# Kernel tuning notes

Hardware: AMD Instinct MI355X
Metric: run time of the kernel (lower is better)

Reference implementation:

```python
import jax, jax.numpy as jnp
import numpy as np

L, H, NH, DH, FF, V = 12, 768, 12, 64, 3072, 21128
B, S, TITLE = 64, 120, 20


def _ln(h, w, b):
    m = h.mean(-1, keepdims=True)
    v = ((h - m) ** 2).mean(-1, keepdims=True)
    return (h - m) * jax.lax.rsqrt(v + 1e-12) * w + b


def _prefix_causal_bias():
    # title tokens attend only to title; content tokens attend to title + causal content
    top = jnp.concatenate([jnp.ones((TITLE, TITLE)), jnp.zeros((TITLE, S - TITLE))], axis=1)
    bot = jnp.concatenate([jnp.ones((S - TITLE, TITLE)), jnp.tril(jnp.ones((S - TITLE, S - TITLE)))], axis=1)
    mask = jnp.concatenate([top, bot], axis=0)  # [S,S]
    return (1.0 - mask) * -1e9


def setup_inputs() -> dict:
    key = jax.random.key(0)
    ks = iter(jax.random.split(key, 32))

    def p(shape):
        return jax.random.normal(next(ks), shape, jnp.float32) * 0.02

    return {
        "x": jax.random.randint(next(ks), (B, S), 0, V),
        "y": jax.random.randint(next(ks), (B, S), 0, V),
        "word_emb": p((V, H)),
        "pos_emb": p((S, H)),
        "type_emb": p((1, H)),
        "emb_ln_w": jnp.ones((H,)), "emb_ln_b": jnp.zeros((H,)),
        "q_w": p((L, H, H)), "q_b": jnp.zeros((L, H)),
        "k_w": p((L, H, H)), "k_b": jnp.zeros((L, H)),
        "v_w": p((L, H, H)), "v_b": jnp.zeros((L, H)),
        "ao_w": p((L, H, H)), "ao_b": jnp.zeros((L, H)),
        "a_ln_w": jnp.ones((L, H)), "a_ln_b": jnp.zeros((L, H)),
        "f1_w": p((L, H, FF)), "f1_b": jnp.zeros((L, FF)),
        "f2_w": p((L, FF, H)), "f2_b": jnp.zeros((L, H)),
        "f_ln_w": jnp.ones((L, H)), "f_ln_b": jnp.zeros((L, H)),
        "cls_w": p((H, V)), "cls_b": jnp.zeros((V,)),
    }


def reference(x, y, word_emb, pos_emb, type_emb, emb_ln_w, emb_ln_b,
              q_w, q_b, k_w, k_b, v_w, v_b, ao_w, ao_b, a_ln_w, a_ln_b,
              f1_w, f1_b, f2_w, f2_b, f_ln_w, f_ln_b, cls_w, cls_b):
    bias = _prefix_causal_bias()[None, None]  # [1,1,S,S]
    h = _ln(word_emb[x] + pos_emb[None] + type_emb[0][None, None], emb_ln_w, emb_ln_b)

    def layer(h, pl):
        qw, qb, kw, kb, vw, vb, aow, aob, alw, alb, f1w, f1b, f2w, f2b, flw, flb = pl
        q = (h @ qw + qb).reshape(B, S, NH, DH)
        k = (h @ kw + kb).reshape(B, S, NH, DH)
        v = (h @ vw + vb).reshape(B, S, NH, DH)
        scores = jnp.einsum('bqhd,bkhd->bhqk', q, k) / np.float32(np.sqrt(DH)) + bias
        attn = jax.nn.softmax(scores, axis=-1)
        ctx = jnp.einsum('bhqk,bkhd->bqhd', attn, v).reshape(B, S, H)
        h = _ln(h + ctx @ aow + aob, alw, alb)
        ff = jax.nn.gelu(h @ f1w + f1b, approximate=False) @ f2w + f2b
        h = _ln(h + ff, flw, flb)
        return h, None

    h, _ = jax.lax.scan(layer, h, (q_w, q_b, k_w, k_b, v_w, v_b, ao_w, ao_b,
                                   a_ln_w, a_ln_b, f1_w, f1_b, f2_w, f2_b,
                                   f_ln_w, f_ln_b))
    logits = h @ cls_w + cls_b  # [B,S,V]
    logp = jax.nn.log_softmax(logits, axis=-1)
    nll = -jnp.take_along_axis(logp, y[..., None], axis=-1)[..., 0]
    return nll.mean()  # torch cross_entropy default reduction='mean'
```

## Files before the change

### kernel.cpp

```cpp
#include <hip/hip_runtime.h>
#include <hip/hip_bf16.h>
#include <hip/hip_fp16.h>
#include <cstdio>
#include <cstdint>

typedef __hip_bfloat16 bf16;
using bf16x8 = __attribute__((ext_vector_type(8))) __bf16;
using f32x4  = __attribute__((ext_vector_type(4))) float;

#define LNUM 12
#define HDIM 768
#define NHEAD 12
#define DHEAD 64
#define FFDIM 3072
#define VOCAB 21128
#define VPAD  21248
#define NBATCH 64
#define SEQ 120
#define TITLEN 20
#define MROWS (NBATCH*SEQ)
#define NTCLS (VPAD/128)

__device__ __forceinline__ float us2f(unsigned short u) {
  union { unsigned int u; float f; } c; c.u = ((unsigned int)u) << 16; return c.f;
}
__device__ __forceinline__ unsigned short f2us(float x) {
  bf16 h = __float2bfloat16(x);
  return *reinterpret_cast<unsigned short*>(&h);
}

template<int EPI>
__launch_bounds__(256, 4)
__global__ void gemm_bt(const bf16* __restrict__ A, const bf16* __restrict__ Bt,
                        const float* __restrict__ bias, bf16* __restrict__ C,
                        int N, int K, int nbx, int nby) {
  __shared__ __align__(16) unsigned short smA[2][128*32];
  __shared__ __align__(16) unsigned short smB[2][128*32];

  const int nwg = nbx * nby;
  const int orig = blockIdx.x;
  const int q8 = nwg >> 3, r8 = nwg & 7;
  const int xcd = orig & 7, lin = orig >> 3;
  const int pid = (xcd < r8 ? xcd * (q8 + 1) : r8 * (q8 + 1) + (xcd - r8) * q8) + lin;
  const int pg = 8 * nbx;
  const int g = pid / pg;
  const int rem = pid - g * pg;
  const int rows = min(8, nby - g * 8);
  const int by = g * 8 + rem % rows;
  const int bx = rem / rows;

  const int t = threadIdx.x;
  const int l = t & 63, w = t >> 6;
  const int wr = w >> 1, wc = w & 1;
  const int brow = by * 128;
  const int bcol = bx * 128;

  f32x4 acc[4][4];
#pragma unroll
  for (int i = 0; i < 4; ++i)
#pragma unroll
    for (int j = 0; j < 4; ++j) acc[i][j] = (f32x4){0.f, 0.f, 0.f, 0.f};

  const int srow = t >> 2;
  const int scol = ((t & 3) ^ ((t >> 3) & 3)) * 8;
  const bf16* gA0 = A  + (size_t)(brow + srow) * K + scol;
  const bf16* gA1 = gA0 + (size_t)64 * K;
  const bf16* gB0 = Bt + (size_t)(bcol + srow) * K + scol;
  const bf16* gB1 = gB0 + (size_t)64 * K;

  const int arow = l & 15;
  const int aslot = (l >> 4) ^ ((arow >> 1) & 3);
  const int aoff = (wr*64 + arow)*32 + aslot*8;
  const int boff = (wc*64 + arow)*32 + aslot*8;

  auto stage = [&](int buf, int k0) {
    __builtin_amdgcn_global_load_lds((const __attribute__((address_space(1))) void*)(gA0 + k0),
                                     (__attribute__((address_space(3))) void*)(smA[buf] + w*512), 16, 0, 0);
    __builtin_amdgcn_global_load_lds((const __attribute__((address_space(1))) void*)(gA1 + k0),
                                     (__attribute__((address_space(3))) void*)(smA[buf] + 2048 + w*512), 16, 0, 0);
    __builtin_amdgcn_global_load_lds((const __attribute__((address_space(1))) void*)(gB0 + k0),
                                     (__attribute__((address_space(3))) void*)(smB[buf] + w*512), 16, 0, 0);
    __builtin_amdgcn_global_load_lds((const __attribute__((address_space(1))) void*)(gB1 + k0),
                                     (__attribute__((address_space(3))) void*)(smB[buf] + 2048 + w*512), 16, 0, 0);
  };

  const int nk = K >> 5;
  stage(0, 0);
  stage(1, 32);

  for (int kt = 0; kt < nk; ++kt) {
    const int sl = kt & 1;
    if (kt + 1 < nk) asm volatile("s_waitcnt vmcnt(4)" ::: "memory");
    else             asm volatile("s_waitcnt vmcnt(0)" ::: "memory");
    __builtin_amdgcn_s_barrier();

    const unsigned short* sa = smA[sl] + aoff;
    const unsigned short* sb = smB[sl] + boff;
    bf16x8 af[4], bg[4];
#pragma unroll
    for (int i = 0; i < 4; ++i) {
      af[i] = *reinterpret_cast<const bf16x8*>(sa + i*512);
      bg[i] = *reinterpret_cast<const bf16x8*>(sb + i*512);
    }
    asm volatile("s_waitcnt lgkmcnt(0)" ::: "memory");
    __builtin_amdgcn_s_barrier();
    if (kt + 2 < nk) stage(sl, (kt + 2) << 5);
    __builtin_amdgcn_sched_barrier(0);

    __builtin_amdgcn_s_setprio(1);
#pragma unroll
    for (int i = 0; i < 4; ++i)
#pragma unroll
      for (int j = 0; j < 4; ++j)
        acc[i][j] = __builtin_amdgcn_mfma_f32_16x16x32_bf16(af[i], bg[j], acc[i][j], 0, 0, 0);
    __builtin_amdgcn_s_setprio(0);
    __builtin_amdgcn_sched_barrier(0);
  }

#pragma unroll
  for (int i = 0; i < 4; ++i) {
    const int row = brow + wr*64 + i*16 + (l >> 4)*4;
#pragma unroll
    for (int j = 0; j < 4; ++j) {
      const int col = bcol + wc*64 + j*16 + (l & 15);
      const float bv = bias[col];
#pragma unroll
      for (int r = 0; r < 4; ++r) {
        float v = acc[i][j][r] + bv;
        if (EPI == 1) v = 0.5f * v * (1.0f + erff(v * 0.70710678118f));
        C[(size_t)(row + r) * N + col] = __float2bfloat16(v);
      }
    }
  }
}

__launch_bounds__(512, 2)
__global__ void gemm_cls8(const bf16* __restrict__ A, const bf16* __restrict__ Bt,
                          const float* __restrict__ bias, float2* __restrict__ parts,
                          int K, int nbx, int nby) {
  __shared__ __align__(16) unsigned short lds[4][2][2][4096];

  const int nwg = nbx * nby;
  const int orig = blockIdx.x;
  const int q8 = nwg >> 3, r8 = nwg & 7;
  const int xcd = orig & 7, lin = orig >> 3;
  const int pid = (xcd < r8 ? xcd * (q8 + 1) : r8 * (q8 + 1) + (xcd - r8) * q8) + lin;
  const int pg = 8 * nbx;
  const int g = pid / pg;
  const int rem = pid - g * pg;
  const int rows = min(8, nby - g * 8);
  const int by = g * 8 + rem % rows;
  const int bx = rem / rows;

  const int t = threadIdx.x;
  const int l = t & 63, w = t >> 6;
  const int wm = w >> 2, wn = w & 3;
  const int brow = by * 256;
  const int bcol = bx * 256;

  f32x4 acc[8][4];
#pragma unroll
  for (int m = 0; m < 8; ++m)
#pragma unroll
    for (int n = 0; n < 4; ++n) acc[m][n] = (f32x4){0.f, 0.f, 0.f, 0.f};

  const int srow = t >> 2;
  const int scol = ((t & 3) ^ ((t >> 3) & 3)) * 8;
  const bf16* gA0 = A  + (size_t)(brow + srow) * K + scol;
  const bf16* gA1 = A  + (size_t)(brow + 128 + srow) * K + scol;
  const bf16* gB0 = Bt + (size_t)(bcol + srow) * K + scol;
  const bf16* gB1 = Bt + (size_t)(bcol + 128 + srow) * K + scol;

  const int arow = l & 15;
  const int aslot = (l >> 4) ^ ((arow >> 1) & 3);
  const int afrag = arow*32 + aslot*8;
  const int bfrag = ((wn & 1)*64 + arow)*32 + aslot*8;

  auto stageA = [&](int rb, int k0) {
    __builtin_amdgcn_global_load_lds((const __attribute__((address_space(1))) void*)(gA0 + k0),
        (__attribute__((address_space(3))) void*)(&lds[rb][0][0][0] + w*512), 16, 0, 0);
    __builtin_amdgcn_global_load_lds((const __attribute__((address_space(1))) void*)(gA1 + k0),
        (__attribute__((address_space(3))) void*)(&lds[rb][0][1][0] + w*512), 16, 0, 0);
  };
  auto stageB = [&](int rb, int k0) {
    __builtin_amdgcn_global_load_lds((const __attribute__((address_space(1))) void*)(gB0 + k0),
        (__attribute__((address_space(3))) void*)(&lds[rb][1][0][0] + w*512), 16, 0, 0);
    __builtin_amdgcn_global_load_lds((const __attribute__((address_space(1))) void*)(gB1 + k0),
        (__attribute__((address_space(3))) void*)(&lds[rb][1][1][0] + w*512), 16, 0, 0);
  };

  const int nk = K >> 5;
  stageA(0, 0);   stageB(0, 0);
  stageA(1, 32);  stageB(1, 32);
  stageA(2, 64);  stageB(2, 64);

  for (int T = 0; T < nk; ++T) {
    const int rb = T & 3;
    if (T + 2 < nk)      asm volatile("s_waitcnt vmcnt(8)" ::: "memory");
    else if (T + 1 < nk) asm volatile("s_waitcnt vmcnt(4)" ::: "memory");
    else                 asm volatile("s_waitcnt vmcnt(0)" ::: "memory");
    __builtin_amdgcn_s_barrier();

    const unsigned short* sa = &lds[rb][0][wm][0] + afrag;
    const unsigned short* sb = &lds[rb][1][wn >> 1][0] + bfrag;

    bf16x8 af[8], bg[4];
#pragma unroll
    for (int m = 0; m < 4; ++m) af[m] = *reinterpret_cast<const bf16x8*>(sa + m*512);
#pragma unroll
    for (int n = 0; n < 4; ++n) bg[n] = *reinterpret_cast<const bf16x8*>(sb + n*512);
    if (T + 3 < nk) stageA((T + 3) & 3, (T + 3) << 5);
    asm volatile("s_waitcnt lgkmcnt(0)" ::: "memory");
    __builtin_amdgcn_sched_barrier(0);
    __builtin_amdgcn_s_setprio(1);
#pragma unroll
    for (int m = 0; m < 4; ++m)
#pragma unroll
      for (int n = 0; n < 4; ++n)
        acc[m][n] = __builtin_amdgcn_mfma_f32_16x16x32_bf16(af[m], bg[n], acc[m][n], 0, 0, 0);
    __builtin_amdgcn_s_setprio(0);
    __builtin_amdgcn_s_barrier();

#pragma unroll
    for (int m = 4; m < 8; ++m) af[m] = *reinterpret_cast<const bf16x8*>(sa + m*512);
    if (T + 3 < nk) stageB((T + 3) & 3, (T + 3) << 5);
    asm volatile("s_waitcnt lgkmcnt(0)" ::: "memory");
    __builtin_amdgcn_sched_barrier(0);
    __builtin_amdgcn_s_setprio(1);
#pragma unroll
    for (int m = 4; m < 8; ++m)
#pragma unroll
      for (int n = 0; n < 4; ++n)
        acc[m][n] = __builtin_amdgcn_mfma_f32_16x16x32_bf16(af[m], bg[n], acc[m][n], 0, 0, 0);
    __builtin_amdgcn_s_setprio(0);
  }

  __syncthreads();
  float* redm = reinterpret_cast<float*>(lds);
  float* reds = redm + 1024;
  float b4[4];
#pragma unroll
  for (int n = 0; n < 4; ++n) b4[n] = bias[bcol + wn*64 + n*16 + (l & 15)];
  float vmax[8][4];
#pragma unroll
  for (int m = 0; m < 8; ++m)
#pragma unroll
    for (int r = 0; r < 4; ++r) {
      float mx = -3.0e38f;
#pragma unroll
      for (int n = 0; n < 4; ++n) mx = fmaxf(mx, acc[m][n][r] + b4[n]);
#pragma unroll
      for (int s = 1; s < 16; s <<= 1) mx = fmaxf(mx, __shfl_xor(mx, s));
      vmax[m][r] = mx;
    }
  if ((l & 15) == 0)
#pragma unroll
    for (int m = 0; m < 8; ++m)
#pragma unroll
      for (int r = 0; r < 4; ++r)
        redm[(wm*128 + m*16 + (l>>4)*4 + r)*4 + wn] = vmax[m][r];
  __syncthreads();
  const int pr = wn >> 1;
  float gmax[8][4], vsum[8][4];
#pragma unroll
  for (int m = 0; m < 8; ++m)
#pragma unroll
    for (int r = 0; r < 4; ++r) {
      const int rl = m*16 + (l>>4)*4 + r;
      const float gm = fmaxf(redm[(wm*128 + rl)*4 + pr*2], redm[(wm*128 + rl)*4 + pr*2 + 1]);
      gmax[m][r] = gm;
      float ss = 0.f;
#pragma unroll
      for (int n = 0; n < 4; ++n) ss += __expf(acc[m][n][r] + b4[n] - gm);
#pragma unroll
      for (int s = 1; s < 16; s <<= 1) ss += __shfl_xor(ss, s);
      vsum[m][r] = ss;
    }
  if ((l & 15) == 0)
#pragma unroll
    for (int m = 0; m < 8; ++m)
#pragma unroll
      for (int r = 0; r < 4; ++r)
        reds[(wm*128 + m*16 + (l>>4)*4 + r)*4 + wn] = vsum[m][r];
  __syncthreads();
  if ((wn & 1) == 0 && (l & 15) == 0)
#pragma unroll
    for (int m = 0; m < 8; ++m)
#pragma unroll
      for (int r = 0; r < 4; ++r) {
        const int rl = m*16 + (l>>4)*4 + r;
        const int row = brow + wm*128 + rl;
        parts[(size_t)row * NTCLS + bx*2 + pr] =
            make_float2(gmax[m][r], reds[(wm*128 + rl)*4 + wn] + reds[(wm*128 + rl)*4 + wn + 1]);
      }
}

__launch_bounds__(256, 2)
__global__ void attn_mfma(const bf16* __restrict__ qkv, bf16* __restrict__ ctx) {
  const int bh = blockIdx.x;
  const int b = bh / NHEAD, h = bh % NHEAD;
  __shared__ __align__(16) unsigned char smem[81920];
  unsigned short* Qs = reinterpret_cast<unsigned short*>(smem);
  unsigned short* Ks = reinterpret_cast<unsigned short*>(smem + 16384);
  unsigned short* Vt = reinterpret_cast<unsigned short*>(smem + 32768);

  const int t = threadIdx.x;
  const int l = t & 63, w = t >> 6;

  const float4 z4 = make_float4(0.f, 0.f, 0.f, 0.f);
#pragma unroll
  for (int rd = 0; rd < 4; ++rd)
    *reinterpret_cast<float4*>(smem + 32768 + (rd*256 + t)*16) = z4;
  if (t < 128) {
    const int mtx = t >> 6;
    const int sl = t & 63;
    *reinterpret_cast<float4*>(smem + mtx*16384 + (960 + sl)*16) = z4;
  }
  __syncthreads();

  const bf16* qbase = qkv + (size_t)(b*SEQ)*2304 + h*DHEAD;
#pragma unroll
  for (int rd = 0; rd < 4; ++rd) {
    const int idx = rd*256 + t;
    if (idx < 960) {
      const int row = idx >> 3, slot = idx & 7;
      const int srccol = (slot ^ (row & 7)) * 8;
      const bf16* src = qbase + (size_t)row*2304 + srccol;
      __builtin_amdgcn_global_load_lds((const __attribute__((address_space(1))) void*)(src),
          (__attribute__((address_space(3))) void*)(Qs + idx*8), 16, 0, 0);
      __builtin_amdgcn_global_load_lds((const __attribute__((address_space(1))) void*)(src + HDIM),
          (__attribute__((address_space(3))) void*)(Ks + idx*8), 16, 0, 0);
    }
  }
#pragma unroll
  for (int rd = 0; rd < 4; ++rd) {
    const int e = rd*256 + t;
    if (e < 960) {
      const int j = e >> 3, d8 = (e & 7) * 8;
      bf16x8 vv = *reinterpret_cast<const bf16x8*>(qbase + (size_t)j*2304 + 2*HDIM + d8);
      const int cs = j >> 3;
#pragma unroll
      for (int q = 0; q < 8; ++q) {
        const int d = d8 + q;
        Vt[d*128 + ((cs ^ (d & 7))*8) + (j & 7)] =
            reinterpret_cast<const unsigned short*>(&vv)[q];
      }
    }
  }
  __syncthreads();

  f32x4 sacc[2][8];
#pragma unroll
  for (int rt = 0; rt < 2; ++rt)
#pragma unroll
    for (int ct = 0; ct < 8; ++ct) sacc[rt][ct] = (f32x4){0.f, 0.f, 0.f, 0.f};

#pragma unroll
  for (int ks = 0; ks < 2; ++ks) {
    const int kslot = (l >> 4) + 4*ks;
    bf16x8 aq[2];
#pragma unroll
    for (int rt = 0; rt < 2; ++rt) {
      const int row = w*32 + rt*16 + (l & 15);
      aq[rt] = *reinterpret_cast<const bf16x8*>(Qs + row*64 + ((kslot ^ (row & 7))*8));
    }
#pragma unroll
    for (int ct = 0; ct < 8; ++ct) {
      const int rk = ct*16 + (l & 15);
      bf16x8 bk = *reinterpret_cast<const bf16x8*>(Ks + rk*64 + ((kslot ^ (rk & 7))*8));
#pragma unroll
      for (int rt = 0; rt < 2; ++rt)
        sacc[rt][ct] = __builtin_amdgcn_mfma_f32_16x16x32_bf16(aq[rt], bk, sacc[rt][ct], 0, 0, 0);
    }
  }

  unsigned short* Pw = reinterpret_cast<unsigned short*>(smem + 49152 + w*8192);
  float rinv[2][4];
#pragma unroll
  for (int rt = 0; rt < 2; ++rt) {
#pragma unroll
    for (int r = 0; r < 4; ++r) {
      const int i = w*32 + rt*16 + (l >> 4)*4 + r;
      float sv[8];
      float best = -3.0e38f;
#pragma unroll
      for (int ct = 0; ct < 8; ++ct) {
        const int j = ct*16 + (l & 15);
        const bool ok = (j < SEQ) && ((i < TITLEN) ? (j < TITLEN) : (j < TITLEN || j <= i));
        sv[ct] = ok ? sacc[rt][ct][r] * 0.125f : -1e30f;
        best = fmaxf(best, sv[ct]);
      }
#pragma unroll
      for (int m = 1; m < 16; m <<= 1) best = fmaxf(best, __shfl_xor(best, m));
      float ss = 0.f;
      const int rowl = rt*16 + (l >> 4)*4 + r;
#pragma unroll
      for (int ct = 0; ct < 8; ++ct) {
        const float p = __expf(sv[ct] - best);
        ss += p;
        const int col = ct*16 + (l & 15);
        const int cs = col >> 3;
        Pw[rowl*128 + ((cs ^ (rowl & 7))*8) + (col & 7)] = f2us(p);
      }
#pragma unroll
      for (int m = 1; m < 16; m <<= 1) ss += __shfl_xor(ss, m);
      rinv[rt][r] = 1.0f / ss;
    }
  }
  asm volatile("s_waitcnt lgkmcnt(0)" ::: "memory");
  __builtin_amdgcn_sched_barrier(0);

  f32x4 oacc[2][4];
#pragma unroll
  for (int rt = 0; rt < 2; ++rt)
#pragma unroll
    for (int dt = 0; dt < 4; ++dt) oacc[rt][dt] = (f32x4){0.f, 0.f, 0.f, 0.f};

#pragma unroll
  for (int ks = 0; ks < 4; ++ks) {
    const int kslot = (l >> 4) + 4*ks;
    bf16x8 ap[2];
#pragma unroll
    for (int rt = 0; rt < 2; ++rt) {
      const int rowl = rt*16 + (l & 15);
      ap[rt] = *reinterpret_cast<const bf16x8*>(Pw + rowl*128 + ((kslot ^ (rowl & 7))*8));
    }
#pragma unroll
    for (int dt = 0; dt < 4; ++dt) {
      const int rv = dt*16 + (l & 15);
      bf16x8 bv = *reinterpret_cast<const bf16x8*>(Vt + rv*128 + ((kslot ^ (rv & 7))*8));
#pragma unroll
      for (int rt = 0; rt < 2; ++rt)
        oacc[rt][dt] = __builtin_amdgcn_mfma_f32_16x16x32_bf16(ap[rt], bv, oacc[rt][dt], 0, 0, 0);
    }
  }

  bf16* obase = ctx + (size_t)(b*SEQ)*HDIM + h*DHEAD;
#pragma unroll
  for (int rt = 0; rt < 2; ++rt)
#pragma unroll
    for (int r = 0; r < 4; ++r) {
      const int i = w*32 + rt*16 + (l >> 4)*4 + r;
      if (i < SEQ) {
#pragma unroll
        for (int dt = 0; dt < 4; ++dt) {
          const int d = dt*16 + (l & 15);
          obase[(size_t)i*HDIM + d] = __float2bfloat16(oacc[rt][dt][r] * rinv[rt][r]);
        }
      }
    }
}

__launch_bounds__(64)
__global__ void embed_ln2(const int* __restrict__ x, const float* __restrict__ wemb,
                          const float* __restrict__ pemb, const float* __restrict__ temb,
                          const float* __restrict__ lw, const float* __restrict__ lb,
                          bf16* __restrict__ resid, bf16* __restrict__ hb) {
  const int row = blockIdx.x;
  const int s = row % SEQ;
  const int tok = x[row];
  const int l = threadIdx.x;
  const int c0 = l * 12;
  float v[12]; float sum = 0.f, sq = 0.f;
#pragma unroll
  for (int i = 0; i < 3; ++i) {
    const float4 a = *reinterpret_cast<const float4*>(wemb + (size_t)tok*HDIM + c0 + i*4);
    const float4 b = *reinterpret_cast<const float4*>(pemb + s*HDIM + c0 + i*4);
    const float4 c = *reinterpret_cast<const float4*>(temb + c0 + i*4);
    v[i*4+0] = a.x + b.x + c.x; v[i*4+1] = a.y + b.y + c.y;
    v[i*4+2] = a.z + b.z + c.z; v[i*4+3] = a.w + b.w + c.w;
#pragma unroll
    for (int e = 0; e < 4; ++e) { sum += v[i*4+e]; sq += v[i*4+e]*v[i*4+e]; }
  }
#pragma unroll
  for (int m = 1; m < 64; m <<= 1) { sum += __shfl_xor(sum, m); sq += __shfl_xor(sq, m); }
  const float mean = sum * (1.0f/HDIM);
  const float rs = rsqrtf(sq*(1.0f/HDIM) - mean*mean + 1e-12f);
  unsigned short* rp = (unsigned short*)resid + (size_t)row*HDIM + c0;
  unsigned short* hp = (unsigned short*)hb    + (size_t)row*HDIM + c0;
#pragma unroll
  for (int i = 0; i < 3; ++i) {
    ushort4 o;
    o.x = f2us((v[i*4+0]-mean)*rs*lw[c0+i*4+0] + lb[c0+i*4+0]);
    o.y = f2us((v[i*4+1]-mean)*rs*lw[c0+i*4+1] + lb[c0+i*4+1]);
    o.z = f2us((v[i*4+2]-mean)*rs*lw[c0+i*4+2] + lb[c0+i*4+2]);
    o.w = f2us((v[i*4+3]-mean)*rs*lw[c0+i*4+3] + lb[c0+i*4+3]);
    *reinterpret_cast<ushort4*>(hp + i*4) = o;
    ushort4 ro;
    ro.x = f2us(v[i*4+0]); ro.y = f2us(v[i*4+1]);
    ro.z = f2us(v[i*4+2]); ro.w = f2us(v[i*4+3]);
    *reinterpret_cast<ushort4*>(rp + i*4) = ro;
  }
}

__launch_bounds__(64)
__global__ void res_ln2(bf16* __restrict__ resid, bf16* __restrict__ hb,
                        const bf16* __restrict__ add,
                        const float* __restrict__ lw, const float* __restrict__ lb) {
  const int row = blockIdx.x;
  const int l = threadIdx.x;
  const int c0 = l * 12;
  const unsigned short* rp = (const unsigned short*)resid + (size_t)row*HDIM + c0;
  const unsigned short* ap = (const unsigned short*)add   + (size_t)row*HDIM + c0;
  float v[12]; float sum = 0.f, sq = 0.f;
#pragma unroll
  for (int i = 0; i < 3; ++i) {
    const ushort4 ra = *reinterpret_cast<const ushort4*>(rp + i*4);
    const ushort4 aa = *reinterpret_cast<const ushort4*>(ap + i*4);
    v[i*4+0] = us2f(ra.x) + us2f(aa.x);
    v[i*4+1] = us2f(ra.y) + us2f(aa.y);
    v[i*4+2] = us2f(ra.z) + us2f(aa.z);
    v[i*4+3] = us2f(ra.w) + us2f(aa.w);
#pragma unroll
    for (int e = 0; e < 4; ++e) { sum += v[i*4+e]; sq += v[i*4+e]*v[i*4+e]; }
  }
#pragma unroll
  for (int m = 1; m < 64; m <<= 1) { sum += __shfl_xor(sum, m); sq += __shfl_xor(sq, m); }
  const float mean = sum * (1.0f/HDIM);
  const float rs = rsqrtf(sq*(1.0f/HDIM) - mean*mean + 1e-12f);
  unsigned short* rw = (unsigned short*)resid + (size_t)row*HDIM + c0;
  unsigned short* hp = (unsigned short*)hb    + (size_t)row*HDIM + c0;
#pragma unroll
  for (int i = 0; i < 3; ++i) {
    ushort4 ro;
    ro.x = f2us(v[i*4+0]); ro.y = f2us(v[i*4+1]);
    ro.z = f2us(v[i*4+2]); ro.w = f2us(v[i*4+3]);
    *reinterpret_cast<ushort4*>(rw + i*4) = ro;
    ushort4 o;
    o.x = f2us((v[i*4+0]-mean)*rs*lw[c0+i*4+0] + lb[c0+i*4+0]);
    o.y = f2us((v[i*4+1]-mean)*rs*lw[c0+i*4+1] + lb[c0+i*4+1]);
    o.z = f2us((v[i*4+2]-mean)*rs*lw[c0+i*4+2] + lb[c0+i*4+2]);
    o.w = f2us((v[i*4+3]-mean)*rs*lw[c0+i*4+3] + lb[c0+i*4+3]);
    *reinterpret_cast<ushort4*>(hp + i*4) = o;
  }
}

__device__ __forceinline__ void transpose_block(const float* in, bf16* out,
                                                int K, int N, int bx, int by) {
  __shared__ float tile[32][33];
  const int tx = threadIdx.x, ty = threadIdx.y;
#pragma unroll
  for (int r = 0; r < 32; r += 8)
    tile[ty+r][tx] = in[(size_t)(by + ty + r) * N + bx + tx];
  __syncthreads();
#pragma unroll
  for (int r = 0; r < 32; r += 8)
    out[(size_t)(bx + ty + r) * K + by + tx] = __float2bfloat16(tile[tx][ty+r]);
}

__device__ __forceinline__ void transpose_sel(int id, int lay,
    const float* qw, const float* kw, const float* vw, const float* aow,
    const float* f1w, const float* f2w,
    bf16* wqkvT, bf16* waoT, bf16* wf1T, bf16* wf2T,
    size_t wstride_qkv, size_t wstride_ao, size_t wstride_f) {
  const size_t o768 = (size_t)768*768, of1 = (size_t)768*FFDIM;
  const float* in; bf16* out; int K, N, nbx;
  if (id < 2304) {
    const int z = id / 576; id -= z * 576;
    in = ((z == 0) ? qw : (z == 1) ? kw : (z == 2) ? vw : aow) + (size_t)lay*o768;
    out = (z < 3) ? (wqkvT + (size_t)lay*wstride_qkv + (size_t)z*o768)
                  : (waoT + (size_t)lay*wstride_ao);
    K = 768; N = 768; nbx = 24;
  } else if (id < 4608) {
    id -= 2304; in = f1w + (size_t)lay*of1; out = wf1T + (size_t)lay*wstride_f;
    K = 768; N = 3072; nbx = 96;
  } else {
    id -= 4608; in = f2w + (size_t)lay*of1; out = wf2T + (size_t)lay*wstride_f;
    K = 3072; N = 768; nbx = 24;
  }
  transpose_block(in, out, K, N, (id % nbx) * 32, (id / nbx) * 32);
}

__global__ void transpose_all(const float* qw, const float* kw, const float* vw,
                              const float* aow, const float* f1w, const float* f2w,
                              bf16* wqkvT, bf16* waoT, bf16* wf1T, bf16* wf2T) {
  transpose_sel(blockIdx.x % 6912, blockIdx.x / 6912, qw, kw, vw, aow, f1w, f2w,
                wqkvT, waoT, wf1T, wf2T,
                (size_t)2304*768, (size_t)768*768, (size_t)768*FFDIM);
}

__global__ void transpose_layer(const float* qw, const float* kw, const float* vw,
                                const float* aow, const float* f1w, const float* f2w,
                                bf16* wqkvT, bf16* waoT, bf16* wf1T, bf16* wf2T,
                                int lay) {
  transpose_sel(blockIdx.x, 0, qw + (size_t)lay*768*768, kw + (size_t)lay*768*768,
                vw + (size_t)lay*768*768, aow + (size_t)lay*768*768,
                f1w + (size_t)lay*768*FFDIM, f2w + (size_t)lay*768*FFDIM,
                wqkvT, waoT, wf1T, wf2T, 0, 0, 0);
}

__global__ void transpose_cls(const float* __restrict__ in, bf16* __restrict__ out) {
  __shared__ float tile[32][33];
  const int bx = blockIdx.x*32, by = blockIdx.y*32;
  const int tx = threadIdx.x, ty = threadIdx.y;
#pragma unroll
  for (int r = 0; r < 32; r += 8) {
    const int n = bx + tx;
    tile[ty+r][tx] = (n < VOCAB) ? in[(size_t)(by + ty + r) * VOCAB + n] : 0.f;
  }
  __syncthreads();
#pragma unroll
  for (int r = 0; r < 32; r += 8) {
    const int n = bx + ty + r;
    if (n < VPAD) out[(size_t)n * 768 + by + tx] = __float2bfloat16(tile[tx][ty+r]);
  }
}

__global__ void prep_bias(const float* __restrict__ qb, const float* __restrict__ kb,
                          const float* __restrict__ vb, const float* __restrict__ clsb,
                          float* __restrict__ qkvb, float* __restrict__ clsbp) {
  const int i = blockIdx.x*256 + threadIdx.x;
  if (i < LNUM*2304) {
    const int l = i / 2304, n = i % 2304;
    float v;
    if (n < 768) v = qb[l*768 + n];
    else if (n < 1536) v = kb[l*768 + n - 768];
    else v = vb[l*768 + n - 1536];
    qkvb[i] = v;
  }
  if (i < VPAD) clsbp[i] = (i < VOCAB) ? clsb[i] : -1e9f;
}

__launch_bounds__(64)
__global__ void ce_merge(const float2* __restrict__ parts, const bf16* __restrict__ hb,
                         const bf16* __restrict__ wclsT, const float* __restrict__ clsb,
                         const int* __restrict__ y, float* __restrict__ out) {
  const int row = blockIdx.x;
  const int l = threadIdx.x;
  const int tgt = y[row];
  float tl = 0.f;
  for (int i = l; i < HDIM; i += 64)
    tl += __bfloat162float(hb[(size_t)row*HDIM + i]) * __bfloat162float(wclsT[(size_t)tgt*HDIM + i]);
#pragma unroll
  for (int m = 1; m < 64; m <<= 1) tl += __shfl_xor(tl, m);
  float mx = -3.0e38f;
  for (int i = l; i < NTCLS; i += 64) mx = fmaxf(mx, parts[(size_t)row*NTCLS + i].x);
#pragma unroll
  for (int m = 1; m < 64; m <<= 1) mx = fmaxf(mx, __shfl_xor(mx, m));
  float ss = 0.f;
  for (int i = l; i < NTCLS; i += 64) {
    const float2 p = parts[(size_t)row*NTCLS + i];
    ss += p.y * __expf(p.x - mx);
  }
#pragma unroll
  for (int m = 1; m < 64; m <<= 1) ss += __shfl_xor(ss, m);
  if (l == 0) {
    const float lse = mx + logf(ss);
    atomicAdd(out, (lse - (tl + clsb[tgt])) * (1.0f / MROWS));
  }
}

extern "C" void kernel_launch(void* const* d_in, const int* in_sizes, int n_in,
                              void* d_out, int out_size, void* d_ws, size_t ws_size,
                              hipStream_t stream) {
  const int*   x     = (const int*)d_in[0];
  const int*   y     = (const int*)d_in[1];
  const float* wemb  = (const float*)d_in[2];
  const float* pemb  = (const float*)d_in[3];
  const float* temb  = (const float*)d_in[4];
  const float* elnw  = (const float*)d_in[5];
  const float* elnb  = (const float*)d_in[6];
  const float* qw    = (const float*)d_in[7];
  const float* qb    = (const float*)d_in[8];
  const float* kw    = (const float*)d_in[9];
  const float* kb    = (const float*)d_in[10];
  const float* vw    = (const float*)d_in[11];
  const float* vb    = (const float*)d_in[12];
  const float* aow   = (const float*)d_in[13];
  const float* aob   = (const float*)d_in[14];
  const float* alnw  = (const float*)d_in[15];
  const float* alnb  = (const float*)d_in[16];
  const float* f1w   = (const float*)d_in[17];
  const float* f1b   = (const float*)d_in[18];
  const float* f2w   = (const float*)d_in[19];
  const float* f2b   = (const float*)d_in[20];
  const float* flnw  = (const float*)d_in[21];
  const float* flnb  = (const float*)d_in[22];
  const float* clsw  = (const float*)d_in[23];
  const float* clsb  = (const float*)d_in[24];

  char* p = (char*)d_ws;
  auto alloc = [&](size_t bytes) { char* r = p; p += (bytes + 255) & ~(size_t)255; return r; };
  bf16*  wclsT = (bf16*)alloc((size_t)VPAD*768*2);
  float* qkvb  = (float*)alloc((size_t)LNUM*2304*4);
  float* clsbp = (float*)alloc((size_t)VPAD*4);
  bf16*  resid = (bf16*)alloc((size_t)MROWS*HDIM*2);
  bf16*  hb    = (bf16*)alloc((size_t)MROWS*HDIM*2);
  bf16*  qkv   = (bf16*)alloc((size_t)MROWS*2304*2);
  bf16*  ctxb  = (bf16*)alloc((size_t)MROWS*HDIM*2);
  bf16*  tmp   = (bf16*)alloc((size_t)MROWS*HDIM*2);
  bf16*  ffh   = (bf16*)alloc((size_t)MROWS*FFDIM*2);
  float2* parts = (float2*)alloc((size_t)MROWS*NTCLS*sizeof(float2));

  const size_t sz_qkvT = (size_t)2304*768*2;
  const size_t sz_aoT  = (size_t)768*768*2;
  const size_t sz_fT   = (size_t)768*FFDIM*2;
  const size_t per_layer_w = ((sz_qkvT+255)&~255ULL) + ((sz_aoT+255)&~255ULL)
                           + 2*((sz_fT+255)&~255ULL);
  const size_t fixed = (size_t)(p - (char*)d_ws);
  const bool big = (fixed + (size_t)LNUM * per_layer_w) <= ws_size;
  const int nlw = big ? LNUM : 1;
  bf16* wqkvT = (bf16*)alloc((size_t)nlw * sz_qkvT);
  bf16* waoT  = (bf16*)alloc((size_t)nlw * sz_aoT);
  bf16* wf1T  = (bf16*)alloc((size_t)nlw * sz_fT);
  bf16* wf2T  = (bf16*)alloc((size_t)nlw * sz_fT);
  if ((size_t)(p - (char*)d_ws) > ws_size) {
    fprintf(stderr, "kernel_launch: ws too small (%zu > %zu)\n",
            (size_t)(p - (char*)d_ws), ws_size);
    return;
  }

  hipMemsetAsync(d_out, 0, (size_t)out_size * sizeof(float), stream);
  prep_bias<<<108, 256, 0, stream>>>(qb, kb, vb, clsb, qkvb, clsbp);
  transpose_cls<<<dim3(VPAD/32, 768/32), dim3(32,8), 0, stream>>>(clsw, wclsT);
  if (big)
    transpose_all<<<LNUM*6912, dim3(32,8), 0, stream>>>(qw, kw, vw, aow, f1w, f2w,
                                                        wqkvT, waoT, wf1T, wf2T);
  embed_ln2<<<MROWS, 64, 0, stream>>>(x, wemb, pemb, temb, elnw, elnb, resid, hb);

  for (int l = 0; l < LNUM; ++l) {
    bf16* lqkvT; bf16* laoT; bf16* lf1T; bf16* lf2T;
    if (big) {
      lqkvT = wqkvT + (size_t)l*2304*768;
      laoT  = waoT  + (size_t)l*768*768;
      lf1T  = wf1T  + (size_t)l*768*FFDIM;
      lf2T  = wf2T  + (size_t)l*768*FFDIM;
    } else {
      lqkvT = wqkvT; laoT = waoT; lf1T = wf1T; lf2T = wf2T;
      transpose_layer<<<6912, dim3(32,8), 0, stream>>>(qw, kw, vw, aow, f1w, f2w,
                                                       lqkvT, laoT, lf1T, lf2T, l);
    }

    gemm_bt<0><<<18*60, 256, 0, stream>>>(hb, lqkvT, qkvb + l*2304, qkv,
                                          2304, HDIM, 18, 60);
    attn_mfma<<<NBATCH*NHEAD, 256, 0, stream>>>(qkv, ctxb);
    gemm_bt<0><<<6*60, 256, 0, stream>>>(ctxb, laoT, aob + l*HDIM, tmp,
                                         768, HDIM, 6, 60);
    res_ln2<<<MROWS, 64, 0, stream>>>(resid, hb, tmp, alnw + l*HDIM, alnb + l*HDIM);
    gemm_bt<1><<<24*60, 256, 0, stream>>>(hb, lf1T, f1b + l*FFDIM, ffh,
                                          FFDIM, HDIM, 24, 60);
    gemm_bt<0><<<6*60, 256, 0, stream>>>(ffh, lf2T, f2b + l*HDIM, tmp,
                                         768, FFDIM, 6, 60);
    res_ln2<<<MROWS, 64, 0, stream>>>(resid, hb, tmp, flnw + l*HDIM, flnb + l*HDIM);
  }

  gemm_cls8<<<83*30, 512, 0, stream>>>(hb, wclsT, clsbp, parts, HDIM, 83, 30);
  ce_merge<<<MROWS, 64, 0, stream>>>(parts, hb, wclsT, clsb, y, (float*)d_out);
}
```

Measured before the change: 3.164 ms.

## Use 256x256-tile 8-wave GEMM with 4-stage LDS pipeline for QKV and FF1

Adds a new GEMM kernel with 256x256 output tiles, 512 threads, an XCD-aware grouped block swizzle and a 4-buffer global_load_lds pipeline that splits loads between two MFMA phases. It replaces the 128x128 GEMM for the QKV and FF1 projections to raise operand reuse and cut global/L2 traffic per FLOP. The trade-off is fewer workgroups (270 and 360 blocks), which may underfill the GPU, plus higher register pressure from the 8x4 accumulators.

```diff
diff --git a/kernel.cpp b/kernel.cpp
--- a/kernel.cpp
+++ b/kernel.cpp
@@ -127,6 +127,125 @@
 #pragma unroll
       for (int r = 0; r < 4; ++r) {
         float v = acc[i][j][r] + bv;
+        if (EPI == 1) v = 0.5f * v * (1.0f + erff(v * 0.70710678118f));
+        C[(size_t)(row + r) * N + col] = __float2bfloat16(v);
+      }
+    }
+  }
+}
+
+template<int EPI>
+__launch_bounds__(512, 2)
+__global__ void gemm256st(const bf16* __restrict__ A, const bf16* __restrict__ Bt,
+                          const float* __restrict__ bias, bf16* __restrict__ C,
+                          int N, int K, int nbx, int nby) {
+  __shared__ __align__(16) unsigned short lds[4][2][2][4096];
+
+  const int nwg = nbx * nby;
+  const int orig = blockIdx.x;
+  const int q8 = nwg >> 3, r8 = nwg & 7;
+  const int xcd = orig & 7, lin = orig >> 3;
+  const int pid = (xcd < r8 ? xcd * (q8 + 1) : r8 * (q8 + 1) + (xcd - r8) * q8) + lin;
+  const int pg = 8 * nbx;
+  const int g = pid / pg;
+  const int rem = pid - g * pg;
+  const int rows = min(8, nby - g * 8);
+  const int by = g * 8 + rem % rows;
+  const int bx = rem / rows;
+
+  const int t = threadIdx.x;
+  const int l = t & 63, w = t >> 6;
+  const int wm = w >> 2, wn = w & 3;
+  const int brow = by * 256;
+  const int bcol = bx * 256;
+
+  f32x4 acc[8][4];
+#pragma unroll
+  for (int m = 0; m < 8; ++m)
+#pragma unroll
+    for (int n = 0; n < 4; ++n) acc[m][n] = (f32x4){0.f, 0.f, 0.f, 0.f};
+
+  const int srow = t >> 2;
+  const int scol = ((t & 3) ^ ((t >> 3) & 3)) * 8;
+  const bf16* gA0 = A  + (size_t)(brow + srow) * K + scol;
+  const bf16* gA1 = A  + (size_t)(brow + 128 + srow) * K + scol;
+  const bf16* gB0 = Bt + (size_t)(bcol + srow) * K + scol;
+  const bf16* gB1 = Bt + (size_t)(bcol + 128 + srow) * K + scol;
+
+  const int arow = l & 15;
+  const int aslot = (l >> 4) ^ ((arow >> 1) & 3);
+  const int afrag = arow*32 + aslot*8;
+  const int bfrag = ((wn & 1)*64 + arow)*32 + aslot*8;
+
+  auto stageA = [&](int rb, int k0) {
+    __builtin_amdgcn_global_load_lds((const __attribute__((address_space(1))) void*)(gA0 + k0),
+        (__attribute__((address_space(3))) void*)(&lds[rb][0][0][0] + w*512), 16, 0, 0);
+    __builtin_amdgcn_global_load_lds((const __attribute__((address_space(1))) void*)(gA1 + k0),
+        (__attribute__((address_space(3))) void*)(&lds[rb][0][1][0] + w*512), 16, 0, 0);
+  };
+  auto stageB = [&](int rb, int k0) {
+    __builtin_amdgcn_global_load_lds((const __attribute__((address_space(1))) void*)(gB0 + k0),
+        (__attribute__((address_space(3))) void*)(&lds[rb][1][0][0] + w*512), 16, 0, 0);
+    __builtin_amdgcn_global_load_lds((const __attribute__((address_space(1))) void*)(gB1 + k0),
+        (__attribute__((address_space(3))) void*)(&lds[rb][1][1][0] + w*512), 16, 0, 0);
+  };
+
+  const int nk = K >> 5;
+  stageA(0, 0);   stageB(0, 0);
+  stageA(1, 32);  stageB(1, 32);
+  stageA(2, 64);  stageB(2, 64);
+
+  for (int T = 0; T < nk; ++T) {
+    const int rb = T & 3;
+    if (T + 2 < nk)      asm volatile("s_waitcnt vmcnt(8)" ::: "memory");
+    else if (T + 1 < nk) asm volatile("s_waitcnt vmcnt(4)" ::: "memory");
+    else                 asm volatile("s_waitcnt vmcnt(0)" ::: "memory");
+    __builtin_amdgcn_s_barrier();
+
+    const unsigned short* sa = &lds[rb][0][wm][0] + afrag;
+    const unsigned short* sb = &lds[rb][1][wn >> 1][0] + bfrag;
+
+    bf16x8 af[8], bg[4];
+#pragma unroll
+    for (int m = 0; m < 4; ++m) af[m] = *reinterpret_cast<const bf16x8*>(sa + m*512);
+#pragma unroll
+    for (int n = 0; n < 4; ++n) bg[n] = *reinterpret_cast<const bf16x8*>(sb + n*512);
+    if (T + 3 < nk) stageA((T + 3) & 3, (T + 3) << 5);
+    asm volatile("s_waitcnt lgkmcnt(0)" ::: "memory");
+    __builtin_amdgcn_sched_barrier(0);
+    __builtin_amdgcn_s_setprio(1);
+#pragma unroll
+    for (int m = 0; m < 4; ++m)
+#pragma unroll
+      for (int n = 0; n < 4; ++n)
+        acc[m][n] = __builtin_amdgcn_mfma_f32_16x16x32_bf16(af[m], bg[n], acc[m][n], 0, 0, 0);
+    __builtin_amdgcn_s_setprio(0);
+    __builtin_amdgcn_s_barrier();
+
+#pragma unroll
+    for (int m = 4; m < 8; ++m) af[m] = *reinterpret_cast<const bf16x8*>(sa + m*512);
+    if (T + 3 < nk) stageB((T + 3) & 3, (T + 3) << 5);
+    asm volatile("s_waitcnt lgkmcnt(0)" ::: "memory");
+    __builtin_amdgcn_sched_barrier(0);
+    __builtin_amdgcn_s_setprio(1);
+#pragma unroll
+    for (int m = 4; m < 8; ++m)
+#pragma unroll
+      for (int n = 0; n < 4; ++n)
+        acc[m][n] = __builtin_amdgcn_mfma_f32_16x16x32_bf16(af[m], bg[n], acc[m][n], 0, 0, 0);
+    __builtin_amdgcn_s_setprio(0);
+  }
+
+#pragma unroll
+  for (int m = 0; m < 8; ++m) {
+    const int row = brow + wm*128 + m*16 + (l >> 4)*4;
+#pragma unroll
+    for (int n = 0; n < 4; ++n) {
+      const int col = bcol + wn*64 + n*16 + (l & 15);
+      const float bv = bias[col];
+#pragma unroll
+      for (int r = 0; r < 4; ++r) {
+        float v = acc[m][n][r] + bv;
         if (EPI == 1) v = 0.5f * v * (1.0f + erff(v * 0.70710678118f));
         C[(size_t)(row + r) * N + col] = __float2bfloat16(v);
       }
@@ -731,14 +850,14 @@
                                                        lqkvT, laoT, lf1T, lf2T, l);
     }
 
-    gemm_bt<0><<<18*60, 256, 0, stream>>>(hb, lqkvT, qkvb + l*2304, qkv,
-                                          2304, HDIM, 18, 60);
+    gemm256st<0><<<9*30, 512, 0, stream>>>(hb, lqkvT, qkvb + l*2304, qkv,
+                                           2304, HDIM, 9, 30);
     attn_mfma<<<NBATCH*NHEAD, 256, 0, stream>>>(qkv, ctxb);
     gemm_bt<0><<<6*60, 256, 0, stream>>>(ctxb, laoT, aob + l*HDIM, tmp,
                                          768, HDIM, 6, 60);
     res_ln2<<<MROWS, 64, 0, stream>>>(resid, hb, tmp, alnw + l*HDIM, alnb + l*HDIM);
-    gemm_bt<1><<<24*60, 256, 0, stream>>>(hb, lf1T, f1b + l*FFDIM, ffh,
-                                          FFDIM, HDIM, 24, 60);
+    gemm256st<1><<<12*30, 512, 0, stream>>>(hb, lf1T, f1b + l*FFDIM, ffh,
+                                            FFDIM, HDIM, 12, 30);
     gemm_bt<0><<<6*60, 256, 0, stream>>>(ffh, lf2T, f2b + l*HDIM, tmp,
                                          768, FFDIM, 6, 60);
     res_ln2<<<MROWS, 64, 0, stream>>>(resid, hb, tmp, flnw + l*HDIM, flnb + l*HDIM);
```

Result: slower. 3.449 ms (+9.0%).
